# Kernel optimization log

Measured on AMD Instinct MI355X. Metric: run time of the kernel, lower is better.

## Reference

```python
import jax, jax.numpy as jnp
import numpy as np

HIDDEN = 1024
HEADS = 16
HEAD_DIM = HIDDEN // HEADS
MAX_SEQ = 2048
BATCH = 2
SEQ = 2048


def setup_inputs() -> dict:
    key = jax.random.key(0)
    ks = jax.random.split(key, 6)
    x = jax.random.normal(ks[0], (BATCH, SEQ, HIDDEN), dtype=jnp.float32)
    # torch Linear params expressed as [in, out] weight + bias
    W1 = jax.random.normal(ks[1], (HIDDEN, 4 * HIDDEN), dtype=jnp.float32) * (HIDDEN ** -0.5)
    b1 = jnp.zeros((4 * HIDDEN,), dtype=jnp.float32)
    W2 = jax.random.normal(ks[2], (HIDDEN, HIDDEN), dtype=jnp.float32) * (HIDDEN ** -0.5)
    b2 = jnp.zeros((HIDDEN,), dtype=jnp.float32)
    rel_table = jax.random.normal(ks[3], (2 * MAX_SEQ - 1, HEADS), dtype=jnp.float32) * 0.02
    # causal mask [B, S, S]; True = keep
    attn_mask = jnp.broadcast_to(jnp.tril(jnp.ones((SEQ, SEQ), dtype=bool)), (BATCH, SEQ, SEQ))
    return {"x": x, "W1": W1, "b1": b1, "W2": W2, "b2": b2,
            "rel_table": rel_table, "attn_mask": attn_mask}


def reference(x, W1, b1, W2, b2, rel_table, attn_mask):
    B, S, H = x.shape
    # fused projection + SiLU, then chunk into U, Q, K, V
    activated = jax.nn.silu(jnp.einsum('bsh,hf->bsf', x, W1) + b1)
    U, Qp, Kp, Vp = jnp.split(activated, 4, axis=-1)
    # [B, nH, S, hd]
    def heads(t):
        return t.reshape(B, S, HEADS, HEAD_DIM).transpose(0, 2, 1, 3)
    Q, K, V = heads(Qp), heads(Kp), heads(Vp)
    scale = HEAD_DIM ** -0.5
    scores = jnp.einsum('bnqd,bnkd->bnqk', Q, K) * scale
    # relative position bias gather: idx[i,j] = i - j + MAX_SEQ - 1
    pos = jnp.arange(S)
    rel_idx = pos[:, None] - pos[None, :] + (MAX_SEQ - 1)  # [S, S]
    rel_bias = rel_table[rel_idx].transpose(2, 0, 1)[None]  # [1, nH, S, S]
    scores = scores + rel_bias
    attn = jax.nn.silu(scores)
    attn = jnp.where(attn_mask[:, None, :, :], attn, 0.0)
    out = jnp.einsum('bnqk,bnkd->bnqd', attn, V)
    out = out.transpose(0, 2, 1, 3).reshape(B, S, H)
    gated = out * U
    return jnp.einsum('bsh,hf->bsf', gated, W2) + b2
```

## Files before the change

### kernel.cpp

```cpp
#include <hip/hip_runtime.h>
#include <hip/hip_bf16.h>
#include <math.h>

#define HIDDEN   1024
#define HEADS    16
#define HEAD_DIM 64
#define SEQ      2048
#define BATCH    2
#define FDIM     4096
#define MTOT     4096
#define MAXSEQ   2048

typedef __bf16 bf16x8 __attribute__((ext_vector_type(8)));
typedef float  f32x4  __attribute__((ext_vector_type(4)));
typedef unsigned short u16;

__device__ __forceinline__ float silu_fast(float v) {
    return v * __builtin_amdgcn_rcpf(1.f + __expf(-v));
}

__device__ __forceinline__ u16 f2bf(float f) {
    union { float f; unsigned u; } v; v.f = f;
    unsigned r = v.u + 0x7FFFu + ((v.u >> 16) & 1u);
    return (u16)(r >> 16);
}
__device__ __forceinline__ float bf2f(u16 b) {
    union { unsigned u; float f; } v; v.u = ((unsigned)b) << 16;
    return v.f;
}
__device__ __forceinline__ unsigned pk2(float a, float b) {
    union { __hip_bfloat162 h; unsigned u; } z;
    z.h = __float22bfloat162_rn(make_float2(a, b));
    return z.u;
}

__device__ __forceinline__ void gload16(const void* g, void* l) {
    __builtin_amdgcn_global_load_lds(
        (const __attribute__((address_space(1))) void*)g,
        (__attribute__((address_space(3))) void*)l, 16, 0, 0);
}

__global__ __launch_bounds__(256) void prep_kernel(
    const float* __restrict__ X, const float* __restrict__ W1,
    const float* __restrict__ W2,
    u16* __restrict__ Xb, u16* __restrict__ W1t, u16* __restrict__ W2t,
    unsigned* __restrict__ ticket)
{
    __shared__ u16 T[64][72];
    const int tid = threadIdx.x;
    const int bid = blockIdx.x;

    if (bid == 0 && tid < 8) ticket[tid] = 0u;

    if (bid < 2048) {
        int idx = (bid * 256 + tid) * 8;
        float4 a = *(const float4*)&X[idx];
        float4 b = *(const float4*)&X[idx + 4];
        uint4 pk = make_uint4(pk2(a.x, a.y), pk2(a.z, a.w),
                              pk2(b.x, b.y), pk2(b.z, b.w));
        *(uint4*)&Xb[idx] = pk;
        return;
    }

    const float* W; u16* Wt; int rows, cols, r0, c0;
    if (bid < 3072) {
        int t = bid - 2048;
        W = W1; Wt = W1t; rows = HIDDEN; cols = FDIM;
        c0 = (t & 63) * 64; r0 = (t >> 6) * 64;
    } else {
        int t = bid - 3072;
        W = W2; Wt = W2t; rows = HIDDEN; cols = HIDDEN;
        c0 = (t & 15) * 64; r0 = (t >> 4) * 64;
    }
#pragma unroll
    for (int l = 0; l < 4; ++l) {
        int idx = tid + l * 256;
        int row = idx >> 4;
        int c4  = (idx & 15) * 4;
        float4 v = *(const float4*)&W[(size_t)(r0 + row) * cols + c0 + c4];
        T[c4 + 0][row] = f2bf(v.x);
        T[c4 + 1][row] = f2bf(v.y);
        T[c4 + 2][row] = f2bf(v.z);
        T[c4 + 3][row] = f2bf(v.w);
    }
    __syncthreads();
#pragma unroll
    for (int l = 0; l < 2; ++l) {
        int idx = tid + l * 256;
        int row = idx >> 3;
        int cb  = (idx & 7) * 8;
        *(float4*)&Wt[(size_t)(c0 + row) * rows + r0 + cb] = *(float4*)&T[row][cb];
    }
}

#define GEMM_CORE(A_PTR, BT_PTR, KDIM, BM_, BN_, WMW, WNW)                     \
    enum { MTI = (BM_) / (WMW) / 16, NTI = (BN_) / (WNW) / 16,                 \
           ACH = (BM_) / 8, BCH = (BN_) / 8 };                                 \
    __shared__ __align__(16) u16 As[(BM_) * 64];                               \
    __shared__ __align__(16) u16 Bs[(BN_) * 64];                               \
    const int tid  = threadIdx.x;                                              \
    const int lane = tid & 63;                                                 \
    const int w    = tid >> 6;                                                 \
    const int wm   = w % (WMW), wn = w / (WMW);                                \
    const int l16  = lane & 15, quad = lane >> 4;                              \
    const int m0   = blockIdx.y * (BM_);                                       \
    const int n0   = blockIdx.x * (BN_);                                       \
    const int srow = lane >> 3;                                                \
    const int scol = (((lane & 7) ^ srow)) * 8;     \
    const int xr   = l16 & 7;                           \
    f32x4 acc[MTI][NTI];                                                       \
    _Pragma("unroll")                                                          \
    for (int mt = 0; mt < MTI; ++mt)                                           \
        _Pragma("unroll")                                                      \
        for (int nt = 0; nt < NTI; ++nt)                                       \
            acc[mt][nt] = (f32x4){0.f, 0.f, 0.f, 0.f};                         \
    for (int k0 = 0; k0 < (KDIM); k0 += 64) {                                  \
        __syncthreads();                                                       \
        _Pragma("unroll")                                                      \
        for (int ci = w; ci < ACH; ci += 4) {                                  \
            unsigned off = __builtin_amdgcn_readfirstlane(ci * 1024);          \
            gload16(&(A_PTR)[(size_t)(m0 + ci * 8 + srow) * (KDIM) + k0 + scol],\
                    (char*)As + off);                                          \
        }                                                                      \
        _Pragma("unroll")                                                      \
        for (int ci = w; ci < BCH; ci += 4) {                                  \
            unsigned off = __builtin_amdgcn_readfirstlane(ci * 1024);          \
            gload16(&(BT_PTR)[(size_t)(n0 + ci * 8 + srow) * (KDIM) + k0 + scol],\
                    (char*)Bs + off);                                          \
        }                                                                      \
        __syncthreads();                                                       \
        _Pragma("unroll")                                                      \
        for (int kc = 0; kc < 2; ++kc) {                                       \
            bf16x8 af[MTI], bfr[NTI];                                          \
            const int gsw = ((kc * 4 + quad) ^ xr) * 8;                        \
            _Pragma("unroll")                                                  \
            for (int t = 0; t < MTI; ++t)                                      \
                af[t]  = *(const bf16x8*)&As[(wm * (BM_ / WMW) + t * 16 + l16) \
                                             * 64 + gsw];                      \
            _Pragma("unroll")                                                  \
            for (int t = 0; t < NTI; ++t)                                      \
                bfr[t] = *(const bf16x8*)&Bs[(wn * (BN_ / WNW) + t * 16 + l16) \
                                             * 64 + gsw];                      \
            _Pragma("unroll")                                                  \
            for (int mt = 0; mt < MTI; ++mt)                                   \
                _Pragma("unroll")                                              \
                for (int nt = 0; nt < NTI; ++nt)                               \
                    acc[mt][nt] = __builtin_amdgcn_mfma_f32_16x16x32_bf16(     \
                        bfr[nt], af[mt], acc[mt][nt], 0, 0, 0);                \
        }                                                                      \
    }

__global__ __launch_bounds__(256, 4) void gemm1_mfma_kernel(
    const u16* __restrict__ A, const u16* __restrict__ Bt,
    const float* __restrict__ b1,
    u16* __restrict__ Ub, u16* __restrict__ Qh,
    u16* __restrict__ Kh, u16* __restrict__ Vh)
{
    GEMM_CORE(A, Bt, HIDDEN, 128, 128, 2, 2)

    const int chunk = n0 >> 10;
    u16* dstbase = (chunk == 0) ? Ub : (chunk == 1) ? Qh : (chunk == 2) ? Kh : Vh;
    const float postscale = (chunk == 1) ? 0.125f : 1.0f;

    float4 bias4[NTI]; int nloc[NTI];
#pragma unroll
    for (int nt = 0; nt < NTI; ++nt) {
        int nb = n0 + wn * 64 + nt * 16 + quad * 4;
        bias4[nt] = *(const float4*)&b1[nb];
        nloc[nt] = nb & 1023;
    }
#pragma unroll
    for (int mt = 0; mt < MTI; ++mt) {
        int m  = m0 + wm * 64 + mt * 16 + l16;
        int bb = m >> 11, s = m & 2047;
#pragma unroll
        for (int nt = 0; nt < NTI; ++nt) {
            float v0 = silu_fast(acc[mt][nt][0] + bias4[nt].x) * postscale;
            float v1 = silu_fast(acc[mt][nt][1] + bias4[nt].y) * postscale;
            float v2 = silu_fast(acc[mt][nt][2] + bias4[nt].z) * postscale;
            float v3 = silu_fast(acc[mt][nt][3] + bias4[nt].w) * postscale;
            uint2 pk = make_uint2(pk2(v0, v1), pk2(v2, v3));
            size_t o;
            if (chunk == 0) {
                o = (size_t)m * 1024 + nloc[nt];
            } else {
                int h = nloc[nt] >> 6, d = nloc[nt] & 63;
                o = (size_t)(((bb * HEADS + h) * SEQ) + s) * HEAD_DIM + d;
            }
            *(uint2*)&dstbase[o] = pk;
        }
    }
}

__global__ __launch_bounds__(256) void gemm2_mfma_kernel(
    const u16* __restrict__ A, const u16* __restrict__ Bt,
    const float* __restrict__ b2, float* __restrict__ Out)
{
    GEMM_CORE(A, Bt, HIDDEN, 64, 64, 2, 2)

    float4 bias4[NTI]; int nb[NTI];
#pragma unroll
    for (int nt = 0; nt < NTI; ++nt) {
        nb[nt] = n0 + wn * 32 + nt * 16 + quad * 4;
        bias4[nt] = *(const float4*)&b2[nb[nt]];
    }
#pragma unroll
    for (int mt = 0; mt < MTI; ++mt) {
        int m = m0 + wm * 32 + mt * 16 + l16;
#pragma unroll
        for (int nt = 0; nt < NTI; ++nt) {
            float4 vv;
            vv.x = acc[mt][nt][0] + bias4[nt].x;
            vv.y = acc[mt][nt][1] + bias4[nt].y;
            vv.z = acc[mt][nt][2] + bias4[nt].z;
            vv.w = acc[mt][nt][3] + bias4[nt].w;
            *(float4*)&Out[(size_t)m * 1024 + nb[nt]] = vv;
        }
    }
}

__global__ __launch_bounds__(256, 3) void attn_mfma_kernel(
    const u16* __restrict__ Qh, const u16* __restrict__ Kh,
    const u16* __restrict__ Vh, const float* __restrict__ rel,
    const u16* __restrict__ Ub, u16* __restrict__ G,
    unsigned* __restrict__ ticket)
{
    __shared__ __align__(16) u16 Ks[128][72];
    __shared__ __align__(16) u16 Vt[64][136];
    __shared__ __align__(16) u16 Ps[2][64][64];
    __shared__ float rel_sh[192];
    __shared__ unsigned sh_t;

    const int tid  = threadIdx.x;
    const int lane = tid & 63;
    const int w    = tid >> 6;
    const int quad = lane >> 4;
    const int l16  = lane & 15;
    const int ws   = w & 1;
    const int pp   = w >> 1;
    const int qbase = ws * 32;
    const int xk   = l16 & 7;
    const int qid  = blockIdx.x & 7;

    const int k_r = tid >> 3,       k_c = (tid & 7) * 8;
    const int v_k = (tid & 31) * 2, v_d = (tid >> 5) * 8;

    for (;;) {
        if (tid == 0) sh_t = atomicAdd(&ticket[qid], 1u);
        __syncthreads();
        const unsigned t = sh_t;
        if (t >= 128u) return;

        const int qt = 31 - (int)(t >> 2);
        const int bh = qid * 4 + (int)(t & 3u);
        const int h  = bh & 15;
        const int bb = bh >> 4;
        const int q0 = qt * 64;

        const u16* Kg = Kh + (size_t)((bb * HEADS + h) * SEQ) * HEAD_DIM;
        const u16* Vg = Vh + (size_t)((bb * HEADS + h) * SEQ) * HEAD_DIM;
        const u16* Qg = Qh + (size_t)((bb * HEADS + h) * SEQ + q0) * HEAD_DIM;

        bf16x8 qa[2][2];
#pragma unroll
        for (int sub = 0; sub < 2; ++sub) {
            const int qr = qbase + sub * 16 + l16;
            qa[sub][0] = *(const bf16x8*)&Qg[qr * HEAD_DIM + quad * 8];
            qa[sub][1] = *(const bf16x8*)&Qg[qr * HEAD_DIM + 32 + quad * 8];
        }

        float4 kA0 = *(const float4*)&Kg[(size_t)k_r * 64 + k_c];
        float4 kA1 = *(const float4*)&Kg[(size_t)(k_r + 32) * 64 + k_c];
        float4 vA0 = *(const float4*)&Vg[(size_t)v_k * 64 + v_d];
        float4 vA1 = *(const float4*)&Vg[(size_t)(v_k + 1) * 64 + v_d];
        float4 kB0, kB1, vB0, vB1;
        if (qt >= 1) {
            kB0 = *(const float4*)&Kg[(size_t)(64 + k_r) * 64 + k_c];
            kB1 = *(const float4*)&Kg[(size_t)(64 + k_r + 32) * 64 + k_c];
            vB0 = *(const float4*)&Vg[(size_t)(64 + v_k) * 64 + v_d];
            vB1 = *(const float4*)&Vg[(size_t)(64 + v_k + 1) * 64 + v_d];
        }
        float relreg = 0.f;
        if (tid < 191) relreg = rel[(size_t)(q0 + 1920 + tid) * HEADS + h];

        f32x4 o[2][4];
#pragma unroll
        for (int sub = 0; sub < 2; ++sub)
#pragma unroll
            for (int dt = 0; dt < 4; ++dt) o[sub][dt] = (f32x4){0.f, 0.f, 0.f, 0.f};

        for (int ip = 0; 2 * ip <= qt; ++ip) {
            const int kp = ip * 128;
            const bool hasB = (2 * ip + 1 <= qt);

            *(float4*)&Ks[k_r][k_c]      = kA0;
            *(float4*)&Ks[k_r + 32][k_c] = kA1;
            {
                union { float4 f; u16 u[8]; } a0, a1;
                a0.f = vA0; a1.f = vA1;
#pragma unroll
                for (int i = 0; i < 8; ++i)
                    *(unsigned*)&Vt[v_d + i][v_k] =
                        (unsigned)a0.u[i] | ((unsigned)a1.u[i] << 16);
            }
            if (hasB) {
                *(float4*)&Ks[64 + k_r][k_c]      = kB0;
                *(float4*)&Ks[64 + k_r + 32][k_c] = kB1;
                union { float4 f; u16 u[8]; } a0, a1;
                a0.f = vB0; a1.f = vB1;
#pragma unroll
                for (int i = 0; i < 8; ++i)
                    *(unsigned*)&Vt[v_d + i][64 + v_k] =
                        (unsigned)a0.u[i] | ((unsigned)a1.u[i] << 16);
            }
            if (tid < 191) rel_sh[tid] = relreg;
            __syncthreads();

            {
                const int nk0 = 2 * ip + 2;
                if (nk0 <= qt) {
                    const int b0 = nk0 * 64;
                    kA0 = *(const float4*)&Kg[(size_t)(b0 + k_r) * 64 + k_c];
                    kA1 = *(const float4*)&Kg[(size_t)(b0 + k_r + 32) * 64 + k_c];
                    vA0 = *(const float4*)&Vg[(size_t)(b0 + v_k) * 64 + v_d];
                    vA1 = *(const float4*)&Vg[(size_t)(b0 + v_k + 1) * 64 + v_d];
                    if (tid < 191)
                        relreg = rel[(size_t)(q0 - kp - 128 + 1920 + tid) * HEADS + h];
                    if (nk0 + 1 <= qt) {
                        const int b1 = b0 + 64;
                        kB0 = *(const float4*)&Kg[(size_t)(b1 + k_r) * 64 + k_c];
                        kB1 = *(const float4*)&Kg[(size_t)(b1 + k_r + 32) * 64 + k_c];
                        vB0 = *(const float4*)&Vg[(size_t)(b1 + v_k) * 64 + v_d];
                        vB1 = *(const float4*)&Vg[(size_t)(b1 + v_k + 1) * 64 + v_d];
                    }
                }
            }

            const int myc = 2 * ip + pp;
            if (myc <= qt) {
                const int ko      = pp * 64;
                const int relofs  = pp ? 63 : 127;
                const bool diag   = (myc == qt);
                const int qrelb   = q0 - kp - ko;

#pragma unroll
                for (int ct = 0; ct < 4; ++ct) {
                    bf16x8 ka0 = *(const bf16x8*)&Ks[ko + ct * 16 + l16][quad * 8];
                    bf16x8 ka1 = *(const bf16x8*)&Ks[ko + ct * 16 + l16][32 + quad * 8];
#pragma unroll
                    for (int sub = 0; sub < 2; ++sub) {
                        f32x4 sc = {0.f, 0.f, 0.f, 0.f};
                        sc = __builtin_amdgcn_mfma_f32_16x16x32_bf16(ka0, qa[sub][0], sc, 0, 0, 0);
                        sc = __builtin_amdgcn_mfma_f32_16x16x32_bf16(ka1, qa[sub][1], sc, 0, 0, 0);
                        const int qrow = qbase + sub * 16 + l16;
                        const int ib   = qrow - ct * 16 - quad * 4 + relofs;
                        float p4[4];
                        if (diag) {
#pragma unroll
                            for (int r = 0; r < 4; ++r) {
                                float s = sc[r] + rel_sh[ib - r];
                                int kloc = ct * 16 + quad * 4 + r;
                                p4[r] = (qrelb + qrow - kloc >= 0) ? silu_fast(s) : 0.f;
                            }
                        } else {
#pragma unroll
                            for (int r = 0; r < 4; ++r) {
                                float s = sc[r] + rel_sh[ib - r];
                                p4[r] = silu_fast(s);
                            }
                        }
                        const int col = (((2 * ct + (quad >> 1)) ^ xk) << 3) + (quad & 1) * 4;
                        *(uint2*)&Ps[pp][qrow][col] =
                            make_uint2(pk2(p4[0], p4[1]), pk2(p4[2], p4[3]));
                    }
                }

                bf16x8 pa0[2], pa1[2];
#pragma unroll
                for (int sub = 0; sub < 2; ++sub) {
                    const int qrow = qbase + sub * 16 + l16;
                    pa0[sub] = *(const bf16x8*)&Ps[pp][qrow][(quad ^ xk) * 8];
                    pa1[sub] = *(const bf16x8*)&Ps[pp][qrow][((4 + quad) ^ xk) * 8];
                }
#pragma unroll
                for (int dt = 0; dt < 4; ++dt) {
                    bf16x8 vb0 = *(const bf16x8*)&Vt[dt * 16 + l16][ko + quad * 8];
                    bf16x8 vb1 = *(const bf16x8*)&Vt[dt * 16 + l16][ko + 32 + quad * 8];
#pragma unroll
                    for (int sub = 0; sub < 2; ++sub) {
                        o[sub][dt] = __builtin_amdgcn_mfma_f32_16x16x32_bf16(pa0[sub], vb0, o[sub][dt], 0, 0, 0);
                        o[sub][dt] = __builtin_amdgcn_mfma_f32_16x16x32_bf16(pa1[sub], vb1, o[sub][dt], 0, 0, 0);
                    }
                }
            }
            __syncthreads();
        }

        float* Ored = (float*)&Ks[0][0];
        if (pp == 1) {
#pragma unroll
            for (int sub = 0; sub < 2; ++sub)
#pragma unroll
                for (int dt = 0; dt < 4; ++dt)
                    *(f32x4*)&Ored[((ws << 3) + (sub << 2) + dt) * 256 + lane * 4] =
                        o[sub][dt];
        }
        __syncthreads();
        if (pp == 0) {
#pragma unroll
            for (int sub = 0; sub < 2; ++sub)
#pragma unroll
                for (int dt = 0; dt < 4; ++dt) {
                    f32x4 r4 = *(const f32x4*)&Ored[((ws << 3) + (sub << 2) + dt) * 256 + lane * 4];
                    o[sub][dt] += r4;
#pragma unroll
                    for (int r = 0; r < 4; ++r) {
                        int q = q0 + qbase + sub * 16 + quad * 4 + r;
                        size_t base = (size_t)(bb * SEQ + q) * HIDDEN +
                                      h * HEAD_DIM + dt * 16 + l16;
                        float u = bf2f(Ub[base]);
                        G[base] = f2bf(o[sub][dt][r] * u);
                    }
                }
        }
    }
}

extern "C" void kernel_launch(void* const* d_in, const int* in_sizes, int n_in,
                              void* d_out, int out_size, void* d_ws, size_t ws_size,
                              hipStream_t stream)
{
    const float* X   = (const float*)d_in[0];
    const float* W1  = (const float*)d_in[1];
    const float* b1  = (const float*)d_in[2];
    const float* W2  = (const float*)d_in[3];
    const float* b2  = (const float*)d_in[4];
    const float* rel = (const float*)d_in[5];
    float* out = (float*)d_out;

    const size_t MH = (size_t)MTOT * HIDDEN;
    u16* Ub   = (u16*)d_ws;
    u16* Qh   = Ub  + MH;
    u16* Kh   = Qh  + MH;
    u16* Vh   = Kh  + MH;
    u16* Gbuf = Vh  + MH;
    u16* Xb   = Gbuf + MH;
    u16* W1t  = Xb  + MH;
    u16* W2t  = W1t + MH;
    unsigned* ticket = (unsigned*)(W2t + (size_t)HIDDEN * HIDDEN);

    prep_kernel<<<3328, 256, 0, stream>>>(X, W1, W2, Xb, W1t, W2t, ticket);
    gemm1_mfma_kernel<<<dim3(FDIM / 128, MTOT / 128), 256, 0, stream>>>(
        Xb, W1t, b1, Ub, Qh, Kh, Vh);
    attn_mfma_kernel<<<dim3(768), 256, 0, stream>>>(
        Qh, Kh, Vh, rel, Ub, Gbuf, ticket);
    gemm2_mfma_kernel<<<dim3(HIDDEN / 64, MTOT / 64), 256, 0, stream>>>(
        Gbuf, W2t, b2, out);
}
```

Before: 231.2 us.

## Fuse GEMM1, attention and GEMM2 into one persistent kernel with grid barriers

Replaces three separate launches (gemm1, attention, gemm2) with a single persistent kernel of 768 blocks. Each phase pulls work tiles from atomic counters, and the phases are separated by spin-wait grid barriers on global counters. Shared memory becomes one arena reused by each phase. This removes launch gaps and per-kernel tail drain, but it needs all 768 blocks resident at once (3 per CU) to avoid deadlock. It also pins GEMM1 to 3 blocks per CU where it previously ran at 4, and the barriers add spin overhead.

```diff
diff --git a/kernel.cpp b/kernel.cpp
--- a/kernel.cpp
+++ b/kernel.cpp
@@ -10,6 +10,7 @@
 #define FDIM     4096
 #define MTOT     4096
 #define MAXSEQ   2048
+#define NBLOCKS  768u
 
 typedef __bf16 bf16x8 __attribute__((ext_vector_type(8)));
 typedef float  f32x4  __attribute__((ext_vector_type(4)));
@@ -40,17 +41,29 @@
         (__attribute__((address_space(3))) void*)l, 16, 0, 0);
 }
 
+__device__ __forceinline__ void grid_gate(unsigned* gate, int tid) {
+    __syncthreads();
+    if (tid == 0) {
+        __threadfence();
+        atomicAdd(gate, 1u);
+        while (atomicAdd(gate, 0u) < NBLOCKS)
+            __builtin_amdgcn_s_sleep(2);
+        __threadfence();
+    }
+    __syncthreads();
+}
+
 __global__ __launch_bounds__(256) void prep_kernel(
     const float* __restrict__ X, const float* __restrict__ W1,
     const float* __restrict__ W2,
     u16* __restrict__ Xb, u16* __restrict__ W1t, u16* __restrict__ W2t,
-    unsigned* __restrict__ ticket)
+    unsigned* __restrict__ slots)
 {
     __shared__ u16 T[64][72];
     const int tid = threadIdx.x;
     const int bid = blockIdx.x;
 
-    if (bid == 0 && tid < 8) ticket[tid] = 0u;
+    if (bid == 0 && tid < 12) slots[tid] = 0u;
 
     if (bid < 2048) {
         int idx = (bid * 256 + tid) * 8;
@@ -93,21 +106,15 @@
     }
 }
 
-#define GEMM_CORE(A_PTR, BT_PTR, KDIM, BM_, BN_, WMW, WNW)                     \
+#define GEMM_CORE_F(A_PTR, BT_PTR, KDIM, BM_, BN_, WMW, WNW, M0_, N0_, ASP, BSP) \
     enum { MTI = (BM_) / (WMW) / 16, NTI = (BN_) / (WNW) / 16,                 \
            ACH = (BM_) / 8, BCH = (BN_) / 8 };                                 \
-    __shared__ __align__(16) u16 As[(BM_) * 64];                               \
-    __shared__ __align__(16) u16 Bs[(BN_) * 64];                               \
-    const int tid  = threadIdx.x;                                              \
-    const int lane = tid & 63;                                                 \
-    const int w    = tid >> 6;                                                 \
-    const int wm   = w % (WMW), wn = w / (WMW);                                \
-    const int l16  = lane & 15, quad = lane >> 4;                              \
-    const int m0   = blockIdx.y * (BM_);                                       \
-    const int n0   = blockIdx.x * (BN_);                                       \
+    u16* As = (ASP); u16* Bs = (BSP);                                          \
+    const int wm = w % (WMW), wn = w / (WMW);                                  \
+    const int m0 = (M0_), n0 = (N0_);                                          \
     const int srow = lane >> 3;                                                \
-    const int scol = (((lane & 7) ^ srow)) * 8;     \
-    const int xr   = l16 & 7;                           \
+    const int scol = (((lane & 7) ^ srow)) * 8;                                \
+    const int xr   = l16 & 7;                                                  \
     f32x4 acc[MTI][NTI];                                                       \
     _Pragma("unroll")                                                          \
     for (int mt = 0; mt < MTI; ++mt)                                           \
@@ -134,12 +141,12 @@
             bf16x8 af[MTI], bfr[NTI];                                          \
             const int gsw = ((kc * 4 + quad) ^ xr) * 8;                        \
             _Pragma("unroll")                                                  \
-            for (int t = 0; t < MTI; ++t)                                      \
-                af[t]  = *(const bf16x8*)&As[(wm * (BM_ / WMW) + t * 16 + l16) \
+            for (int t2 = 0; t2 < MTI; ++t2)                                   \
+                af[t2]  = *(const bf16x8*)&As[(wm * (BM_ / WMW) + t2 * 16 + l16)\
                                              * 64 + gsw];                      \
             _Pragma("unroll")                                                  \
-            for (int t = 0; t < NTI; ++t)                                      \
-                bfr[t] = *(const bf16x8*)&Bs[(wn * (BN_ / WNW) + t * 16 + l16) \
+            for (int t2 = 0; t2 < NTI; ++t2)                                   \
+                bfr[t2] = *(const bf16x8*)&Bs[(wn * (BN_ / WNW) + t2 * 16 + l16)\
                                              * 64 + gsw];                      \
             _Pragma("unroll")                                                  \
             for (int mt = 0; mt < MTI; ++mt)                                   \
@@ -150,85 +157,17 @@
         }                                                                      \
     }
 
-__global__ __launch_bounds__(256, 4) void gemm1_mfma_kernel(
-    const u16* __restrict__ A, const u16* __restrict__ Bt,
+__global__ __launch_bounds__(256, 3) void fused_kernel(
+    const u16* __restrict__ Xb, const u16* __restrict__ W1t,
     const float* __restrict__ b1,
     u16* __restrict__ Ub, u16* __restrict__ Qh,
-    u16* __restrict__ Kh, u16* __restrict__ Vh)
+    u16* __restrict__ Kh, u16* __restrict__ Vh,
+    const float* __restrict__ rel, u16* __restrict__ G,
+    const u16* __restrict__ W2t, const float* __restrict__ b2,
+    float* __restrict__ Out,
+    unsigned* __restrict__ slots)
 {
-    GEMM_CORE(A, Bt, HIDDEN, 128, 128, 2, 2)
-
-    const int chunk = n0 >> 10;
-    u16* dstbase = (chunk == 0) ? Ub : (chunk == 1) ? Qh : (chunk == 2) ? Kh : Vh;
-    const float postscale = (chunk == 1) ? 0.125f : 1.0f;
-
-    float4 bias4[NTI]; int nloc[NTI];
-#pragma unroll
-    for (int nt = 0; nt < NTI; ++nt) {
-        int nb = n0 + wn * 64 + nt * 16 + quad * 4;
-        bias4[nt] = *(const float4*)&b1[nb];
-        nloc[nt] = nb & 1023;
-    }
-#pragma unroll
-    for (int mt = 0; mt < MTI; ++mt) {
-        int m  = m0 + wm * 64 + mt * 16 + l16;
-        int bb = m >> 11, s = m & 2047;
-#pragma unroll
-        for (int nt = 0; nt < NTI; ++nt) {
-            float v0 = silu_fast(acc[mt][nt][0] + bias4[nt].x) * postscale;
-            float v1 = silu_fast(acc[mt][nt][1] + bias4[nt].y) * postscale;
-            float v2 = silu_fast(acc[mt][nt][2] + bias4[nt].z) * postscale;
-            float v3 = silu_fast(acc[mt][nt][3] + bias4[nt].w) * postscale;
-            uint2 pk = make_uint2(pk2(v0, v1), pk2(v2, v3));
-            size_t o;
-            if (chunk == 0) {
-                o = (size_t)m * 1024 + nloc[nt];
-            } else {
-                int h = nloc[nt] >> 6, d = nloc[nt] & 63;
-                o = (size_t)(((bb * HEADS + h) * SEQ) + s) * HEAD_DIM + d;
-            }
-            *(uint2*)&dstbase[o] = pk;
-        }
-    }
-}
-
-__global__ __launch_bounds__(256) void gemm2_mfma_kernel(
-    const u16* __restrict__ A, const u16* __restrict__ Bt,
-    const float* __restrict__ b2, float* __restrict__ Out)
-{
-    GEMM_CORE(A, Bt, HIDDEN, 64, 64, 2, 2)
-
-    float4 bias4[NTI]; int nb[NTI];
-#pragma unroll
-    for (int nt = 0; nt < NTI; ++nt) {
-        nb[nt] = n0 + wn * 32 + nt * 16 + quad * 4;
-        bias4[nt] = *(const float4*)&b2[nb[nt]];
-    }
-#pragma unroll
-    for (int mt = 0; mt < MTI; ++mt) {
-        int m = m0 + wm * 32 + mt * 16 + l16;
-#pragma unroll
-        for (int nt = 0; nt < NTI; ++nt) {
-            float4 vv;
-            vv.x = acc[mt][nt][0] + bias4[nt].x;
-            vv.y = acc[mt][nt][1] + bias4[nt].y;
-            vv.z = acc[mt][nt][2] + bias4[nt].z;
-            vv.w = acc[mt][nt][3] + bias4[nt].w;
-            *(float4*)&Out[(size_t)m * 1024 + nb[nt]] = vv;
-        }
-    }
-}
-
-__global__ __launch_bounds__(256, 3) void attn_mfma_kernel(
-    const u16* __restrict__ Qh, const u16* __restrict__ Kh,
-    const u16* __restrict__ Vh, const float* __restrict__ rel,
-    const u16* __restrict__ Ub, u16* __restrict__ G,
-    unsigned* __restrict__ ticket)
-{
-    __shared__ __align__(16) u16 Ks[128][72];
-    __shared__ __align__(16) u16 Vt[64][136];
-    __shared__ __align__(16) u16 Ps[2][64][64];
-    __shared__ float rel_sh[192];
+    __shared__ __align__(16) u16 arena[26624];
     __shared__ unsigned sh_t;
 
     const int tid  = threadIdx.x;
@@ -236,192 +175,283 @@
     const int w    = tid >> 6;
     const int quad = lane >> 4;
     const int l16  = lane & 15;
-    const int ws   = w & 1;
-    const int pp   = w >> 1;
-    const int qbase = ws * 32;
-    const int xk   = l16 & 7;
-    const int qid  = blockIdx.x & 7;
-
-    const int k_r = tid >> 3,       k_c = (tid & 7) * 8;
-    const int v_k = (tid & 31) * 2, v_d = (tid >> 5) * 8;
 
     for (;;) {
-        if (tid == 0) sh_t = atomicAdd(&ticket[qid], 1u);
+        if (tid == 0) sh_t = atomicAdd(&slots[8], 1u);
         __syncthreads();
-        const unsigned t = sh_t;
-        if (t >= 128u) return;
-
-        const int qt = 31 - (int)(t >> 2);
-        const int bh = qid * 4 + (int)(t & 3u);
-        const int h  = bh & 15;
-        const int bb = bh >> 4;
-        const int q0 = qt * 64;
-
-        const u16* Kg = Kh + (size_t)((bb * HEADS + h) * SEQ) * HEAD_DIM;
-        const u16* Vg = Vh + (size_t)((bb * HEADS + h) * SEQ) * HEAD_DIM;
-        const u16* Qg = Qh + (size_t)((bb * HEADS + h) * SEQ + q0) * HEAD_DIM;
-
-        bf16x8 qa[2][2];
-#pragma unroll
-        for (int sub = 0; sub < 2; ++sub) {
-            const int qr = qbase + sub * 16 + l16;
-            qa[sub][0] = *(const bf16x8*)&Qg[qr * HEAD_DIM + quad * 8];
-            qa[sub][1] = *(const bf16x8*)&Qg[qr * HEAD_DIM + 32 + quad * 8];
+        const unsigned tk = sh_t;
+        if (tk >= 1024u) break;
+        {
+            GEMM_CORE_F(Xb, W1t, HIDDEN, 128, 128, 2, 2,
+                        (int)(tk >> 5) * 128, (int)(tk & 31u) * 128,
+                        arena, arena + 8192)
+
+            const int chunk = n0 >> 10;
+            u16* dstbase = (chunk == 0) ? Ub : (chunk == 1) ? Qh
+                         : (chunk == 2) ? Kh : Vh;
+            const float postscale = (chunk == 1) ? 0.125f : 1.0f;
+
+            float4 bias4[NTI]; int nloc[NTI];
+#pragma unroll
+            for (int nt = 0; nt < NTI; ++nt) {
+                int nb = n0 + wn * 64 + nt * 16 + quad * 4;
+                bias4[nt] = *(const float4*)&b1[nb];
+                nloc[nt] = nb & 1023;
+            }
+#pragma unroll
+            for (int mt = 0; mt < MTI; ++mt) {
+                int m  = m0 + wm * 64 + mt * 16 + l16;
+                int bb = m >> 11, s = m & 2047;
+#pragma unroll
+                for (int nt = 0; nt < NTI; ++nt) {
+                    float v0 = silu_fast(acc[mt][nt][0] + bias4[nt].x) * postscale;
+                    float v1 = silu_fast(acc[mt][nt][1] + bias4[nt].y) * postscale;
+                    float v2 = silu_fast(acc[mt][nt][2] + bias4[nt].z) * postscale;
+                    float v3 = silu_fast(acc[mt][nt][3] + bias4[nt].w) * postscale;
+                    uint2 pk = make_uint2(pk2(v0, v1), pk2(v2, v3));
+                    size_t o;
+                    if (chunk == 0) {
+                        o = (size_t)m * 1024 + nloc[nt];
+                    } else {
+                        int h = nloc[nt] >> 6, d = nloc[nt] & 63;
+                        o = (size_t)(((bb * HEADS + h) * SEQ) + s) * HEAD_DIM + d;
+                    }
+                    *(uint2*)&dstbase[o] = pk;
+                }
+            }
         }
-
-        float4 kA0 = *(const float4*)&Kg[(size_t)k_r * 64 + k_c];
-        float4 kA1 = *(const float4*)&Kg[(size_t)(k_r + 32) * 64 + k_c];
-        float4 vA0 = *(const float4*)&Vg[(size_t)v_k * 64 + v_d];
-        float4 vA1 = *(const float4*)&Vg[(size_t)(v_k + 1) * 64 + v_d];
-        float4 kB0, kB1, vB0, vB1;
-        if (qt >= 1) {
-            kB0 = *(const float4*)&Kg[(size_t)(64 + k_r) * 64 + k_c];
-            kB1 = *(const float4*)&Kg[(size_t)(64 + k_r + 32) * 64 + k_c];
-            vB0 = *(const float4*)&Vg[(size_t)(64 + v_k) * 64 + v_d];
-            vB1 = *(const float4*)&Vg[(size_t)(64 + v_k + 1) * 64 + v_d];
+    }
+
+    grid_gate(&slots[10], tid);
+
+    {
+        u16 (*Ks)[72]      = (u16(*)[72])(arena);
+        u16 (*Vt)[136]     = (u16(*)[136])(arena + 9216);
+        u16 (*Ps)[64][64]  = (u16(*)[64][64])(arena + 17920);
+        float* rel_sh      = (float*)(arena + 26112);
+
+        const int ws   = w & 1;
+        const int pp   = w >> 1;
+        const int qbase = ws * 32;
+        const int xk   = l16 & 7;
+        const int qid  = blockIdx.x & 7;
+
+        const int k_r = tid >> 3,       k_c = (tid & 7) * 8;
+        const int v_k = (tid & 31) * 2, v_d = (tid >> 5) * 8;
+
+        for (;;) {
+            if (tid == 0) sh_t = atomicAdd(&slots[qid], 1u);
+            __syncthreads();
+            const unsigned t = sh_t;
+            if (t >= 128u) break;
+
+            const int qt = 31 - (int)(t >> 2);
+            const int bh = qid * 4 + (int)(t & 3u);
+            const int h  = bh & 15;
+            const int bb = bh >> 4;
+            const int q0 = qt * 64;
+
+            const u16* Kg = Kh + (size_t)((bb * HEADS + h) * SEQ) * HEAD_DIM;
+            const u16* Vg = Vh + (size_t)((bb * HEADS + h) * SEQ) * HEAD_DIM;
+            const u16* Qg = Qh + (size_t)((bb * HEADS + h) * SEQ + q0) * HEAD_DIM;
+
+            bf16x8 qa[2][2];
+#pragma unroll
+            for (int sub = 0; sub < 2; ++sub) {
+                const int qr = qbase + sub * 16 + l16;
+                qa[sub][0] = *(const bf16x8*)&Qg[qr * HEAD_DIM + quad * 8];
+                qa[sub][1] = *(const bf16x8*)&Qg[qr * HEAD_DIM + 32 + quad * 8];
+            }
+
+            float4 kA0 = *(const float4*)&Kg[(size_t)k_r * 64 + k_c];
+            float4 kA1 = *(const float4*)&Kg[(size_t)(k_r + 32) * 64 + k_c];
+            float4 vA0 = *(const float4*)&Vg[(size_t)v_k * 64 + v_d];
+            float4 vA1 = *(const float4*)&Vg[(size_t)(v_k + 1) * 64 + v_d];
+            float4 kB0, kB1, vB0, vB1;
+            if (qt >= 1) {
+                kB0 = *(const float4*)&Kg[(size_t)(64 + k_r) * 64 + k_c];
+                kB1 = *(const float4*)&Kg[(size_t)(64 + k_r + 32) * 64 + k_c];
+                vB0 = *(const float4*)&Vg[(size_t)(64 + v_k) * 64 + v_d];
+                vB1 = *(const float4*)&Vg[(size_t)(64 + v_k + 1) * 64 + v_d];
+            }
+            float relreg = 0.f;
+            if (tid < 191) relreg = rel[(size_t)(q0 + 1920 + tid) * HEADS + h];
+
+            f32x4 o[2][4];
+#pragma unroll
+            for (int sub = 0; sub < 2; ++sub)
+#pragma unroll
+                for (int dt = 0; dt < 4; ++dt)
+                    o[sub][dt] = (f32x4){0.f, 0.f, 0.f, 0.f};
+
+            for (int ip = 0; 2 * ip <= qt; ++ip) {
+                const int kp = ip * 128;
+                const bool hasB = (2 * ip + 1 <= qt);
+
+                *(float4*)&Ks[k_r][k_c]      = kA0;
+                *(float4*)&Ks[k_r + 32][k_c] = kA1;
+                {
+                    union { float4 f; u16 u[8]; } a0, a1;
+                    a0.f = vA0; a1.f = vA1;
+#pragma unroll
+                    for (int i = 0; i < 8; ++i)
+                        *(unsigned*)&Vt[v_d + i][v_k] =
+                            (unsigned)a0.u[i] | ((unsigned)a1.u[i] << 16);
+                }
+                if (hasB) {
+                    *(float4*)&Ks[64 + k_r][k_c]      = kB0;
+                    *(float4*)&Ks[64 + k_r + 32][k_c] = kB1;
+                    union { float4 f; u16 u[8]; } a0, a1;
+                    a0.f = vB0; a1.f = vB1;
+#pragma unroll
+                    for (int i = 0; i < 8; ++i)
+                        *(unsigned*)&Vt[v_d + i][64 + v_k] =
+                            (unsigned)a0.u[i] | ((unsigned)a1.u[i] << 16);
+                }
+                if (tid < 191) rel_sh[tid] = relreg;
+                __syncthreads();
+
+                {
+                    const int nk0 = 2 * ip + 2;
+                    if (nk0 <= qt) {
+                        const int b0 = nk0 * 64;
+                        kA0 = *(const float4*)&Kg[(size_t)(b0 + k_r) * 64 + k_c];
+                        kA1 = *(const float4*)&Kg[(size_t)(b0 + k_r + 32) * 64 + k_c];
+                        vA0 = *(const float4*)&Vg[(size_t)(b0 + v_k) * 64 + v_d];
+                        vA1 = *(const float4*)&Vg[(size_t)(b0 + v_k + 1) * 64 + v_d];
+                        if (tid < 191)
+                            relreg = rel[(size_t)(q0 - kp - 128 + 1920 + tid) * HEADS + h];
+                        if (nk0 + 1 <= qt) {
+                            const int b1 = b0 + 64;
+                            kB0 = *(const float4*)&Kg[(size_t)(b1 + k_r) * 64 + k_c];
+                            kB1 = *(const float4*)&Kg[(size_t)(b1 + k_r + 32) * 64 + k_c];
+                            vB0 = *(const float4*)&Vg[(size_t)(b1 + v_k) * 64 + v_d];
+                            vB1 = *(const float4*)&Vg[(size_t)(b1 + v_k + 1) * 64 + v_d];
+                        }
+                    }
+                }
+
+                const int myc = 2 * ip + pp;
+                if (myc <= qt) {
+                    const int ko      = pp * 64;
+                    const int relofs  = pp ? 63 : 127;
+                    const bool diag   = (myc == qt);
+                    const int qrelb   = q0 - kp - ko;
+
+#pragma unroll
+                    for (int ct = 0; ct < 4; ++ct) {
+                        bf16x8 ka0 = *(const bf16x8*)&Ks[ko + ct * 16 + l16][quad * 8];
+                        bf16x8 ka1 = *(const bf16x8*)&Ks[ko + ct * 16 + l16][32 + quad * 8];
+#pragma unroll
+                        for (int sub = 0; sub < 2; ++sub) {
+                            f32x4 sc = {0.f, 0.f, 0.f, 0.f};
+                            sc = __builtin_amdgcn_mfma_f32_16x16x32_bf16(ka0, qa[sub][0], sc, 0, 0, 0);
+                            sc = __builtin_amdgcn_mfma_f32_16x16x32_bf16(ka1, qa[sub][1], sc, 0, 0, 0);
+                            const int qrow = qbase + sub * 16 + l16;
+                            const int ib   = qrow - ct * 16 - quad * 4 + relofs;
+                            float p4[4];
+                            if (diag) {
+#pragma unroll
+                                for (int r = 0; r < 4; ++r) {
+                                    float s = sc[r] + rel_sh[ib - r];
+                                    int kloc = ct * 16 + quad * 4 + r;
+                                    p4[r] = (qrelb + qrow - kloc >= 0) ? silu_fast(s) : 0.f;
+                                }
+                            } else {
+#pragma unroll
+                                for (int r = 0; r < 4; ++r) {
+                                    float s = sc[r] + rel_sh[ib - r];
+                                    p4[r] = silu_fast(s);
+                                }
+                            }
+                            const int col = (((2 * ct + (quad >> 1)) ^ xk) << 3) + (quad & 1) * 4;
+                            *(uint2*)&Ps[pp][qrow][col] =
+                                make_uint2(pk2(p4[0], p4[1]), pk2(p4[2], p4[3]));
+                        }
+                    }
+
+                    bf16x8 pa0[2], pa1[2];
+#pragma unroll
+                    for (int sub = 0; sub < 2; ++sub) {
+                        const int qrow = qbase + sub * 16 + l16;
+                        pa0[sub] = *(const bf16x8*)&Ps[pp][qrow][(quad ^ xk) * 8];
+                        pa1[sub] = *(const bf16x8*)&Ps[pp][qrow][((4 + quad) ^ xk) * 8];
+                    }
+#pragma unroll
+                    for (int dt = 0; dt < 4; ++dt) {
+                        bf16x8 vb0 = *(const bf16x8*)&Vt[dt * 16 + l16][ko + quad * 8];
+                        bf16x8 vb1 = *(const bf16x8*)&Vt[dt * 16 + l16][ko + 32 + quad * 8];
+#pragma unroll
+                        for (int sub = 0; sub < 2; ++sub) {
+                            o[sub][dt] = __builtin_amdgcn_mfma_f32_16x16x32_bf16(pa0[sub], vb0, o[sub][dt], 0, 0, 0);
+                            o[sub][dt] = __builtin_amdgcn_mfma_f32_16x16x32_bf16(pa1[sub], vb1, o[sub][dt], 0, 0, 0);
+                        }
+                    }
+                }
+                __syncthreads();
+            }
+
+            float* Ored = (float*)&Ks[0][0];
+            if (pp == 1) {
+#pragma unroll
+                for (int sub = 0; sub < 2; ++sub)
+#pragma unroll
+                    for (int dt = 0; dt < 4; ++dt)
+                        *(f32x4*)&Ored[((ws << 3) + (sub << 2) + dt) * 256 + lane * 4] =
+                            o[sub][dt];
+            }
+            __syncthreads();
+            if (pp == 0) {
+#pragma unroll
+                for (int sub = 0; sub < 2; ++sub)
+#pragma unroll
+                    for (int dt = 0; dt < 4; ++dt) {
+                        f32x4 r4 = *(const f32x4*)&Ored[((ws << 3) + (sub << 2) + dt) * 256 + lane * 4];
+                        o[sub][dt] += r4;
+#pragma unroll
+                        for (int r = 0; r < 4; ++r) {
+                            int q = q0 + qbase + sub * 16 + quad * 4 + r;
+                            size_t base = (size_t)(bb * SEQ + q) * HIDDEN +
+                                          h * HEAD_DIM + dt * 16 + l16;
+                            float u = bf2f(Ub[base]);
+                            G[base] = f2bf(o[sub][dt][r] * u);
+                        }
+                    }
+            }
         }
-        float relreg = 0.f;
-        if (tid < 191) relreg = rel[(size_t)(q0 + 1920 + tid) * HEADS + h];
-
-        f32x4 o[2][4];
-#pragma unroll
-        for (int sub = 0; sub < 2; ++sub)
-#pragma unroll
-            for (int dt = 0; dt < 4; ++dt) o[sub][dt] = (f32x4){0.f, 0.f, 0.f, 0.f};
-
-        for (int ip = 0; 2 * ip <= qt; ++ip) {
-            const int kp = ip * 128;
-            const bool hasB = (2 * ip + 1 <= qt);
-
-            *(float4*)&Ks[k_r][k_c]      = kA0;
-            *(float4*)&Ks[k_r + 32][k_c] = kA1;
-            {
-                union { float4 f; u16 u[8]; } a0, a1;
-                a0.f = vA0; a1.f = vA1;
-#pragma unroll
-                for (int i = 0; i < 8; ++i)
-                    *(unsigned*)&Vt[v_d + i][v_k] =
-                        (unsigned)a0.u[i] | ((unsigned)a1.u[i] << 16);
-            }
-            if (hasB) {
-                *(float4*)&Ks[64 + k_r][k_c]      = kB0;
-                *(float4*)&Ks[64 + k_r + 32][k_c] = kB1;
-                union { float4 f; u16 u[8]; } a0, a1;
-                a0.f = vB0; a1.f = vB1;
-#pragma unroll
-                for (int i = 0; i < 8; ++i)
-                    *(unsigned*)&Vt[v_d + i][64 + v_k] =
-                        (unsigned)a0.u[i] | ((unsigned)a1.u[i] << 16);
-            }
-            if (tid < 191) rel_sh[tid] = relreg;
-            __syncthreads();
-
-            {
-                const int nk0 = 2 * ip + 2;
-                if (nk0 <= qt) {
-                    const int b0 = nk0 * 64;
-                    kA0 = *(const float4*)&Kg[(size_t)(b0 + k_r) * 64 + k_c];
-                    kA1 = *(const float4*)&Kg[(size_t)(b0 + k_r + 32) * 64 + k_c];
-                    vA0 = *(const float4*)&Vg[(size_t)(b0 + v_k) * 64 + v_d];
-                    vA1 = *(const float4*)&Vg[(size_t)(b0 + v_k + 1) * 64 + v_d];
-                    if (tid < 191)
-                        relreg = rel[(size_t)(q0 - kp - 128 + 1920 + tid) * HEADS + h];
-                    if (nk0 + 1 <= qt) {
-                        const int b1 = b0 + 64;
-                        kB0 = *(const float4*)&Kg[(size_t)(b1 + k_r) * 64 + k_c];
-                        kB1 = *(const float4*)&Kg[(size_t)(b1 + k_r + 32) * 64 + k_c];
-                        vB0 = *(const float4*)&Vg[(size_t)(b1 + v_k) * 64 + v_d];
-                        vB1 = *(const float4*)&Vg[(size_t)(b1 + v_k + 1) * 64 + v_d];
-                    }
-                }
-            }
-
-            const int myc = 2 * ip + pp;
-            if (myc <= qt) {
-                const int ko      = pp * 64;
-                const int relofs  = pp ? 63 : 127;
-                const bool diag   = (myc == qt);
-                const int qrelb   = q0 - kp - ko;
-
-#pragma unroll
-                for (int ct = 0; ct < 4; ++ct) {
-                    bf16x8 ka0 = *(const bf16x8*)&Ks[ko + ct * 16 + l16][quad * 8];
-                    bf16x8 ka1 = *(const bf16x8*)&Ks[ko + ct * 16 + l16][32 + quad * 8];
-#pragma unroll
-                    for (int sub = 0; sub < 2; ++sub) {
-                        f32x4 sc = {0.f, 0.f, 0.f, 0.f};
-                        sc = __builtin_amdgcn_mfma_f32_16x16x32_bf16(ka0, qa[sub][0], sc, 0, 0, 0);
-                        sc = __builtin_amdgcn_mfma_f32_16x16x32_bf16(ka1, qa[sub][1], sc, 0, 0, 0);
-                        const int qrow = qbase + sub * 16 + l16;
-                        const int ib   = qrow - ct * 16 - quad * 4 + relofs;
-                        float p4[4];
-                        if (diag) {
-#pragma unroll
-                            for (int r = 0; r < 4; ++r) {
-                                float s = sc[r] + rel_sh[ib - r];
-                                int kloc = ct * 16 + quad * 4 + r;
-                                p4[r] = (qrelb + qrow - kloc >= 0) ? silu_fast(s) : 0.f;
-                            }
-                        } else {
-#pragma unroll
-                            for (int r = 0; r < 4; ++r) {
-                                float s = sc[r] + rel_sh[ib - r];
-                                p4[r] = silu_fast(s);
-                            }
-                        }
-                        const int col = (((2 * ct + (quad >> 1)) ^ xk) << 3) + (quad & 1) * 4;
-                        *(uint2*)&Ps[pp][qrow][col] =
-                            make_uint2(pk2(p4[0], p4[1]), pk2(p4[2], p4[3]));
-                    }
-                }
-
-                bf16x8 pa0[2], pa1[2];
-#pragma unroll
-                for (int sub = 0; sub < 2; ++sub) {
-                    const int qrow = qbase + sub * 16 + l16;
-                    pa0[sub] = *(const bf16x8*)&Ps[pp][qrow][(quad ^ xk) * 8];
-                    pa1[sub] = *(const bf16x8*)&Ps[pp][qrow][((4 + quad) ^ xk) * 8];
-                }
-#pragma unroll
-                for (int dt = 0; dt < 4; ++dt) {
-                    bf16x8 vb0 = *(const bf16x8*)&Vt[dt * 16 + l16][ko + quad * 8];
-                    bf16x8 vb1 = *(const bf16x8*)&Vt[dt * 16 + l16][ko + 32 + quad * 8];
-#pragma unroll
-                    for (int sub = 0; sub < 2; ++sub) {
-                        o[sub][dt] = __builtin_amdgcn_mfma_f32_16x16x32_bf16(pa0[sub], vb0, o[sub][dt], 0, 0, 0);
-                        o[sub][dt] = __builtin_amdgcn_mfma_f32_16x16x32_bf16(pa1[sub], vb1, o[sub][dt], 0, 0, 0);
-                    }
-                }
-            }
-            __syncthreads();
-        }
-
-        float* Ored = (float*)&Ks[0][0];
-        if (pp == 1) {
-#pragma unroll
-            for (int sub = 0; sub < 2; ++sub)
-#pragma unroll
-                for (int dt = 0; dt < 4; ++dt)
-                    *(f32x4*)&Ored[((ws << 3) + (sub << 2) + dt) * 256 + lane * 4] =
-                        o[sub][dt];
-        }
+    }
+
+    grid_gate(&slots[11], tid);
+
+    for (;;) {
+        if (tid == 0) sh_t = atomicAdd(&slots[9], 1u);
         __syncthreads();
-        if (pp == 0) {
-#pragma unroll
-            for (int sub = 0; sub < 2; ++sub)
-#pragma unroll
-                for (int dt = 0; dt < 4; ++dt) {
-                    f32x4 r4 = *(const f32x4*)&Ored[((ws << 3) + (sub << 2) + dt) * 256 + lane * 4];
-                    o[sub][dt] += r4;
-#pragma unroll
-                    for (int r = 0; r < 4; ++r) {
-                        int q = q0 + qbase + sub * 16 + quad * 4 + r;
-                        size_t base = (size_t)(bb * SEQ + q) * HIDDEN +
-                                      h * HEAD_DIM + dt * 16 + l16;
-                        float u = bf2f(Ub[base]);
-                        G[base] = f2bf(o[sub][dt][r] * u);
-                    }
-                }
+        const unsigned tk = sh_t;
+        if (tk >= 1024u) break;
+        {
+            GEMM_CORE_F(G, W2t, HIDDEN, 64, 64, 2, 2,
+                        (int)(tk >> 4) * 64, (int)(tk & 15u) * 64,
+                        arena, arena + 4096)
+
+            float4 bias4[NTI]; int nb[NTI];
+#pragma unroll
+            for (int nt = 0; nt < NTI; ++nt) {
+                nb[nt] = n0 + wn * 32 + nt * 16 + quad * 4;
+                bias4[nt] = *(const float4*)&b2[nb[nt]];
+            }
+#pragma unroll
+            for (int mt = 0; mt < MTI; ++mt) {
+                int m = m0 + wm * 32 + mt * 16 + l16;
+#pragma unroll
+                for (int nt = 0; nt < NTI; ++nt) {
+                    float4 vv;
+                    vv.x = acc[mt][nt][0] + bias4[nt].x;
+                    vv.y = acc[mt][nt][1] + bias4[nt].y;
+                    vv.z = acc[mt][nt][2] + bias4[nt].z;
+                    vv.w = acc[mt][nt][3] + bias4[nt].w;
+                    *(float4*)&Out[(size_t)m * 1024 + nb[nt]] = vv;
+                }
+            }
         }
     }
 }
@@ -447,13 +477,9 @@
     u16* Xb   = Gbuf + MH;
     u16* W1t  = Xb  + MH;
     u16* W2t  = W1t + MH;
-    unsigned* ticket = (unsigned*)(W2t + (size_t)HIDDEN * HIDDEN);
-
-    prep_kernel<<<3328, 256, 0, stream>>>(X, W1, W2, Xb, W1t, W2t, ticket);
-    gemm1_mfma_kernel<<<dim3(FDIM / 128, MTOT / 128), 256, 0, stream>>>(
-        Xb, W1t, b1, Ub, Qh, Kh, Vh);
-    attn_mfma_kernel<<<dim3(768), 256, 0, stream>>>(
-        Qh, Kh, Vh, rel, Ub, Gbuf, ticket);
-    gemm2_mfma_kernel<<<dim3(HIDDEN / 64, MTOT / 64), 256, 0, stream>>>(
-        Gbuf, W2t, b2, out);
-}
+    unsigned* slots = (unsigned*)(W2t + (size_t)HIDDEN * HIDDEN);
+
+    prep_kernel<<<3328, 256, 0, stream>>>(X, W1, W2, Xb, W1t, W2t, slots);
+    fused_kernel<<<NBLOCKS, 256, 0, stream>>>(
+        Xb, W1t, b1, Ub, Qh, Kh, Vh, rel, Gbuf, W2t, b2, out, slots);
+}
```

Result: slower. 548.1 us (+137.1%).
